# Performance work log

Measured on AMD Instinct MI355X. Metric: run time of the kernel, lower is better.

## Reference

```python
import jax, jax.numpy as jnp
import numpy as np

EPS = 1e-6
LN_EPS = 1e-6

def _mlstm_parallel_stabilized(q, k, v, igate_preact, fgate_preact):
    # q,k,v: (B,NH,S,DH); igate_preact,fgate_preact: (B,NH,S,1)
    B, NH, S, DH = q.shape
    log_fg = jax.nn.log_sigmoid(fgate_preact[..., 0])            # (B,NH,S)
    cs = jnp.cumsum(log_fg, axis=-1)                             # (B,NH,S)
    # log decay matrix: entry (i,j) = cumsum_i - cumsum_j, lower-triangular (j<=i)
    fg_mat = cs[..., :, None] - cs[..., None, :]                 # (B,NH,S,S)
    mask = jnp.tril(jnp.ones((S, S), dtype=bool))
    log_D = jnp.where(mask, fg_mat + igate_preact[..., 0][..., None, :], -jnp.inf)
    max_log_D = jnp.max(log_D, axis=-1, keepdims=True)           # (B,NH,S,1)
    D = jnp.exp(log_D - max_log_D)                               # (B,NH,S,S)
    k_scaled = k / jnp.sqrt(jnp.float32(DH)).astype(k.dtype)
    qk = jnp.einsum('bhsd,bhtd->bhst', q, k_scaled)              # (B,NH,S,S)
    C = qk * D
    normalizer = jnp.maximum(jnp.abs(jnp.sum(C, axis=-1, keepdims=True)), jnp.exp(-max_log_D))
    C_norm = C / (normalizer + EPS)
    return jnp.einsum('bhst,bhtd->bhsd', C_norm, v)              # (B,NH,S,DH)

def _multihead_layernorm(x, weight):
    # x: (B,NH,S,DH), weight: (NH,DH); normalize over DH per head, no bias
    mu = jnp.mean(x, axis=-1, keepdims=True)
    var = jnp.mean(jnp.square(x - mu), axis=-1, keepdims=True)
    xn = (x - mu) * jax.lax.rsqrt(var + LN_EPS)
    return xn * weight[None, :, None, :]

def setup_inputs() -> dict:
    key = jax.random.key(0)
    ks = jax.random.split(key, 6)
    B, S, E, NH = 2, 2048, 1024, 8
    q = jax.random.normal(ks[0], (B, S, E), dtype=jnp.float32)
    k = jax.random.normal(ks[1], (B, S, E), dtype=jnp.float32)
    v = jax.random.normal(ks[2], (B, S, E), dtype=jnp.float32)
    igate_kernel = jnp.zeros((3 * E, NH), dtype=jnp.float32)
    igate_bias = 0.1 * jax.random.normal(ks[3], (NH,), dtype=jnp.float32)
    fgate_kernel = jnp.zeros((3 * E, NH), dtype=jnp.float32)
    fgate_bias = jnp.linspace(3.0, 6.0, NH, dtype=jnp.float32)
    outnorm_weight = jnp.ones((NH, E // NH), dtype=jnp.float32)
    return {"q": q, "k": k, "v": v,
            "igate_kernel": igate_kernel, "igate_bias": igate_bias,
            "fgate_kernel": fgate_kernel, "fgate_bias": fgate_bias,
            "outnorm_weight": outnorm_weight}

def reference(q, k, v, igate_kernel, igate_bias, fgate_kernel, fgate_bias, outnorm_weight):
    B, S, E = q.shape
    NH = igate_bias.shape[0]
    qkv = jnp.concatenate([q, k, v], axis=-1)                    # (B,S,3E)
    igate_preact = qkv @ igate_kernel + igate_bias               # (B,S,NH)
    fgate_preact = qkv @ fgate_kernel + fgate_bias               # (B,S,NH)
    qh = q.reshape(B, S, NH, -1).transpose(0, 2, 1, 3)           # (B,NH,S,DH)
    kh = k.reshape(B, S, NH, -1).transpose(0, 2, 1, 3)
    vh = v.reshape(B, S, NH, -1).transpose(0, 2, 1, 3)
    ig = igate_preact.transpose(0, 2, 1)[..., None]              # (B,NH,S,1)
    fg = fgate_preact.transpose(0, 2, 1)[..., None]
    h = _mlstm_parallel_stabilized(qh, kh, vh, ig, fg)           # (B,NH,S,DH)
    h_norm = _multihead_layernorm(h, outnorm_weight)
    return h_norm.transpose(0, 2, 1, 3).reshape(B, S, -1)        # (B,S,E)
```

## Files before the change

kernel.cpp:

```cpp
#include <hip/hip_runtime.h>
#include <math.h>

#define S_LEN 2048
#define E_DIM 1024
#define NHEAD 8
#define DHEAD 128

typedef short bf16x8 __attribute__((ext_vector_type(8)));
typedef float f32x4 __attribute__((ext_vector_type(4)));
typedef unsigned int u32x4 __attribute__((ext_vector_type(4)));
typedef unsigned int u32x2 __attribute__((ext_vector_type(2)));

constexpr float RSQ_DH  = 0.08838834764831843f;
constexpr float LNRSQ   = -2.4260151319598084f;
constexpr float EPS_NORM = 1e-6f;
constexpr float LN_EPS_C = 1e-6f;

__device__ inline unsigned bfpair(float lo, float hi) {
  unsigned a = __builtin_bit_cast(unsigned, lo);
  unsigned b = __builtin_bit_cast(unsigned, hi);
  a = (a + 0x7fffu + ((a >> 16) & 1u)) >> 16;
  b = (b + 0x7fffu + ((b >> 16) & 1u)) >> 16;
  return a | (b << 16);
}

__device__ inline void gload_lds16(const void* g, void* lds) {
  __builtin_amdgcn_global_load_lds(
      (const __attribute__((address_space(1))) unsigned int*)g,
      (__attribute__((address_space(3))) unsigned int*)lds, 16, 0, 0);
}

__global__ __launch_bounds__(256) void gates_fused(
    const float* __restrict__ q, const float* __restrict__ k, const float* __restrict__ v,
    const float* __restrict__ Wi, const float* __restrict__ bi,
    const float* __restrict__ Wf, const float* __restrict__ bf,
    float* __restrict__ ig_pre, float* __restrict__ fg_pre,
    unsigned short* __restrict__ kb) {
  const int t = threadIdx.x;
  const int row0 = blockIdx.x * 4;
  const int b = row0 >> 11;
  const int s0 = row0 & 2047;
  float p[4][16];
#pragma unroll
  for (int rr = 0; rr < 4; ++rr)
#pragma unroll
    for (int c = 0; c < 16; ++c) p[rr][c] = 0.f;

#pragma unroll
  for (int i = 0; i < 3; ++i) {
    const float* base = (i == 0) ? q : (i == 1) ? k : v;
    float xs[4][4];
#pragma unroll
    for (int rr = 0; rr < 4; ++rr) {
      const float4 xv = *(const float4*)(base + (size_t)(row0 + rr) * E_DIM + t * 4);
      xs[rr][0] = xv.x; xs[rr][1] = xv.y; xs[rr][2] = xv.z; xs[rr][3] = xv.w;
    }
#pragma unroll
    for (int j = 0; j < 4; ++j) {
      const int ge = i * E_DIM + t * 4 + j;
      const float4 wiA = *(const float4*)(Wi + (size_t)ge * 8);
      const float4 wiB = *(const float4*)(Wi + (size_t)ge * 8 + 4);
      const float4 wfA = *(const float4*)(Wf + (size_t)ge * 8);
      const float4 wfB = *(const float4*)(Wf + (size_t)ge * 8 + 4);
      const float wv16[16] = {wiA.x, wiA.y, wiA.z, wiA.w, wiB.x, wiB.y, wiB.z, wiB.w,
                              wfA.x, wfA.y, wfA.z, wfA.w, wfB.x, wfB.y, wfB.z, wfB.w};
#pragma unroll
      for (int rr = 0; rr < 4; ++rr) {
        const float x = xs[rr][j];
#pragma unroll
        for (int c = 0; c < 16; ++c) p[rr][c] += x * wv16[c];
      }
    }
    if (i == 1 && kb != nullptr) {
      const int h = (t * 4) >> 7, d = (t * 4) & 127;
#pragma unroll
      for (int rr = 0; rr < 4; ++rr) {
        u32x2 pk;
        pk.x = bfpair(xs[rr][0], xs[rr][1]);
        pk.y = bfpair(xs[rr][2], xs[rr][3]);
        *(u32x2*)(kb + (((size_t)b * NHEAD + h) * S_LEN + (s0 + rr)) * DHEAD + d) = pk;
      }
    }
  }

#pragma unroll
  for (int rr = 0; rr < 4; ++rr)
#pragma unroll
    for (int c = 0; c < 16; ++c) {
      float val = p[rr][c];
      val += __shfl_xor(val, 1);
      val += __shfl_xor(val, 2);
      val += __shfl_xor(val, 4);
      val += __shfl_xor(val, 8);
      val += __shfl_xor(val, 16);
      val += __shfl_xor(val, 32);
      p[rr][c] = val;
    }
  __shared__ float sred[4][4][16];
  const int wid = t >> 6, lane = t & 63;
  if (lane == 0) {
#pragma unroll
    for (int rr = 0; rr < 4; ++rr)
#pragma unroll
      for (int c = 0; c < 16; ++c) sred[wid][rr][c] = p[rr][c];
  }
  __syncthreads();
  if (t < 64) {
    const int rr = t >> 4, c = t & 15;
    float sum = sred[0][rr][c] + sred[1][rr][c] + sred[2][rr][c] + sred[3][rr][c];
    const int h = c & 7;
    const int row = row0 + rr;
    const int bb = row / S_LEN, s = row % S_LEN;
    if (c < 8) ig_pre[((size_t)bb * NHEAD + h) * S_LEN + s] = sum + bi[h];
    else       fg_pre[((size_t)bb * NHEAD + h) * S_LEN + s] = sum + bf[h];
  }
}

__global__ __launch_bounds__(256) void vtrans(const float* __restrict__ v,
                                              unsigned short* __restrict__ vtb) {
  __shared__ unsigned int tile[128][36];
  const int bid = blockIdx.x;
  const int bh = bid >> 5, st = bid & 31;
  const int b = bh >> 3, h = bh & 7;
  const int s0 = st * 64;
  const int t = threadIdx.x;
#pragma unroll
  for (int i = 0; i < 4; ++i) {
    const int task = t + 256 * i;
    const int sp = task & 31, dq = task >> 5;
    const float* src = v + ((size_t)b * S_LEN + s0 + 2 * sp) * E_DIM + h * DHEAD + dq * 4;
    const float4 r0 = *(const float4*)(src);
    const float4 r1 = *(const float4*)(src + E_DIM);
    tile[dq * 4 + 0][sp] = bfpair(r0.x, r1.x);
    tile[dq * 4 + 1][sp] = bfpair(r0.y, r1.y);
    tile[dq * 4 + 2][sp] = bfpair(r0.z, r1.z);
    tile[dq * 4 + 3][sp] = bfpair(r0.w, r1.w);
  }
  __syncthreads();
#pragma unroll
  for (int i = 0; i < 2; ++i) {
    const int task = t + 256 * i;
    const int d = task >> 2, c4 = task & 3;
    u32x4 w0, w1;
    w0.x = tile[d][c4 * 8 + 0]; w0.y = tile[d][c4 * 8 + 1];
    w0.z = tile[d][c4 * 8 + 2]; w0.w = tile[d][c4 * 8 + 3];
    w1.x = tile[d][c4 * 8 + 4]; w1.y = tile[d][c4 * 8 + 5];
    w1.z = tile[d][c4 * 8 + 6]; w1.w = tile[d][c4 * 8 + 7];
    unsigned short* dst = vtb + ((size_t)bh * DHEAD + d) * S_LEN + s0 + c4 * 16;
    *(u32x4*)(dst)     = w0;
    *(u32x4*)(dst + 8) = w1;
  }
}

__global__ __launch_bounds__(256) void scan_kernel(
    const float* __restrict__ ig_pre, const float* __restrict__ fg_pre,
    float* __restrict__ cs_out, float* __restrict__ g_out, float* __restrict__ gmax_out,
    float g_add) {
  const int bhh = blockIdx.x;
  const int t = threadIdx.x;
  const size_t base = (size_t)bhh * S_LEN;
  float vals[8];
  float run = 0.f;
#pragma unroll
  for (int i = 0; i < 8; ++i) {
    const float x = fg_pre[base + t * 8 + i];
    const float lf = fminf(x, 0.f) - log1pf(__expf(-fabsf(x)));
    run += lf;
    vals[i] = run;
  }
  __shared__ float sums[256];
  sums[t] = run;
  __syncthreads();
  for (int off = 1; off < 256; off <<= 1) {
    const float other = (t >= off) ? sums[t - off] : 0.f;
    __syncthreads();
    sums[t] += other;
    __syncthreads();
  }
  const float prefix = (t > 0) ? sums[t - 1] : 0.f;
  float g_loc[8], gm_loc[8];
  float lmax = -3.4e38f;
#pragma unroll
  for (int i = 0; i < 8; ++i) {
    const float csv = vals[i] + prefix;
    vals[i] = csv;
    const float gg = ig_pre[base + t * 8 + i] - csv;
    g_loc[i] = gg;
    lmax = fmaxf(lmax, gg);
    gm_loc[i] = lmax;
  }
  __shared__ float maxs[256];
  maxs[t] = lmax;
  __syncthreads();
  for (int off = 1; off < 256; off <<= 1) {
    const float other = (t >= off) ? maxs[t - off] : -3.4e38f;
    __syncthreads();
    maxs[t] = fmaxf(maxs[t], other);
    __syncthreads();
  }
  const float pmax = (t > 0) ? maxs[t - 1] : -3.4e38f;
#pragma unroll
  for (int i = 0; i < 8; ++i) {
    cs_out[base + t * 8 + i]   = vals[i];
    g_out[base + t * 8 + i]    = g_loc[i] + g_add;
    gmax_out[base + t * 8 + i] = fmaxf(gm_loc[i], pmax);
  }
}

__global__ __launch_bounds__(128) void mlstm_mfma3(
    const unsigned short* __restrict__ kb, const unsigned short* __restrict__ vtb,
    const float* __restrict__ q,
    const float* __restrict__ cs, const float* __restrict__ garr, const float* __restrict__ gmax,
    const float* __restrict__ wgt, float* __restrict__ out) {
  __shared__ __align__(16) unsigned char kbuf[16384];
  __shared__ __align__(16) unsigned char vbuf[16384];
  __shared__ float g_sh[64];

  const int bid = blockIdx.x;
  const int bh = 2 * (bid & 7) + ((bid >> 3) & 1);
  const int qb = 63 - (bid >> 4);
  const int b = bh >> 3, h = bh & 7;
  const int t = threadIdx.x;
  const int w = t >> 6;
  const int l = t & 63;
  const int r = l & 15;
  const int qq = l >> 4;
  const size_t bhS = (size_t)bh * S_LEN;

  const int gr = qb * 32 + 2 * r + w;
  const float gm_lane = gmax[bhS + gr];

  bf16x8 qfrag[4];
  {
    const float* qrow = q + ((size_t)b * S_LEN + gr) * E_DIM + h * DHEAD;
#pragma unroll
    for (int c = 0; c < 4; ++c) {
      const float4 f0 = *(const float4*)(qrow + 32 * c + 8 * qq);
      const float4 f1 = *(const float4*)(qrow + 32 * c + 8 * qq + 4);
      u32x4 u;
      u.x = bfpair(f0.x, f0.y); u.y = bfpair(f0.z, f0.w);
      u.z = bfpair(f1.x, f1.y); u.w = bfpair(f1.z, f1.w);
      qfrag[c] = __builtin_bit_cast(bf16x8, u);
    }
  }

  f32x4 o[8];
#pragma unroll
  for (int n = 0; n < 8; ++n) o[n] = (f32x4){0.f, 0.f, 0.f, 0.f};
  float den_p = 0.f;

  const unsigned short* kt = kb + bhS * DHEAD;
  const unsigned short* vt = vtb + (size_t)bh * DHEAD * S_LEN;

  const int ntiles = (qb >> 1) + 1;
  for (int jt = 0; jt < ntiles; ++jt) {
    const int j0 = jt * 64;
#pragma unroll
    for (int a = 0; a < 8; ++a) {
      const int m = w * 512 + a * 64 + l;
      const int u = m ^ ((m >> 4) & 7);
      const int j = u >> 4, seg = u & 15;
      gload_lds16(kt + ((size_t)(j0 + j)) * DHEAD + seg * 8,
                  &kbuf[(w * 512 + a * 64) * 16]);
    }
#pragma unroll
    for (int a = 0; a < 8; ++a) {
      const int m = w * 512 + a * 64 + l;
      const int u = m ^ ((m >> 3) & 7);
      const int d = u >> 3, qv = u & 7;
      gload_lds16(vt + (size_t)d * S_LEN + j0 + qv * 8,
                  &vbuf[(w * 512 + a * 64) * 16]);
    }
    if (t < 64) g_sh[t] = garr[bhS + j0 + t];
    asm volatile("s_waitcnt vmcnt(0)" ::: "memory");
    __syncthreads();

    f32x4 st[4];
#pragma unroll
    for (int g = 0; g < 4; ++g) st[g] = (f32x4){0.f, 0.f, 0.f, 0.f};
#pragma unroll
    for (int c = 0; c < 4; ++c) {
#pragma unroll
      for (int g = 0; g < 4; ++g) {
        const int u = ((16 * g + r) * 16 + 4 * c + qq) ^ (r & 7);
        bf16x8 ka = *(const bf16x8*)&kbuf[u * 16];
        st[g] = __builtin_amdgcn_mfma_f32_16x16x32_bf16(ka, qfrag[c], st[g], 0, 0, 0);
      }
    }

    const bool diag = (jt == ntiles - 1);
    unsigned P[4][2];
#pragma unroll
    for (int g = 0; g < 4; ++g) {
      float wv[4];
#pragma unroll
      for (int m = 0; m < 4; ++m) {
        const int jl = 16 * g + 4 * qq + m;
        float ww = st[g][m] * __expf(g_sh[jl] - gm_lane);
        if (diag && (j0 + jl > gr)) ww = 0.f;
        wv[m] = ww;
        den_p += ww;
      }
      P[g][0] = bfpair(wv[0], wv[1]);
      P[g][1] = bfpair(wv[2], wv[3]);
    }

    unsigned A0[4], A1[4];
#pragma unroll
    for (int m = 0; m < 4; ++m) {
      const int srcl = r + 16 * (2 * (qq & 1) + (m >> 1));
      const unsigned x0 = (unsigned)__shfl((int)P[0][m & 1], srcl);
      const unsigned x1 = (unsigned)__shfl((int)P[1][m & 1], srcl);
      const unsigned x2 = (unsigned)__shfl((int)P[2][m & 1], srcl);
      const unsigned x3 = (unsigned)__shfl((int)P[3][m & 1], srcl);
      A0[m] = (qq < 2) ? x0 : x1;
      A1[m] = (qq < 2) ? x2 : x3;
    }
    u32x4 ua0, ua1;
    ua0.x = A0[0]; ua0.y = A0[1]; ua0.z = A0[2]; ua0.w = A0[3];
    ua1.x = A1[0]; ua1.y = A1[1]; ua1.z = A1[2]; ua1.w = A1[3];
    const bf16x8 pa0 = __builtin_bit_cast(bf16x8, ua0);
    const bf16x8 pa1 = __builtin_bit_cast(bf16x8, ua1);

#pragma unroll
    for (int n = 0; n < 8; ++n) {
      const int d = 16 * n + r;
      const int u0 = (d * 8 + qq)     ^ (d & 7);
      const int u1 = (d * 8 + 4 + qq) ^ (d & 7);
      bf16x8 vb0 = *(const bf16x8*)&vbuf[u0 * 16];
      bf16x8 vb1 = *(const bf16x8*)&vbuf[u1 * 16];
      o[n] = __builtin_amdgcn_mfma_f32_16x16x32_bf16(pa0, vb0, o[n], 0, 0, 0);
      o[n] = __builtin_amdgcn_mfma_f32_16x16x32_bf16(pa1, vb1, o[n], 0, 0, 0);
    }
    __syncthreads();
  }

  float den_f = den_p;
  den_f += __shfl_xor(den_f, 16);
  den_f += __shfl_xor(den_f, 32);

  const float* wrow = wgt + h * DHEAD;
  float wv_n[8];
#pragma unroll
  for (int n = 0; n < 8; ++n) wv_n[n] = wrow[16 * n + r];

#pragma unroll
  for (int m = 0; m < 4; ++m) {
    const int iloc = 4 * qq + m;
    const float den_o = __shfl(den_f, iloc);
    const int grow = qb * 32 + 2 * iloc + w;
    const float csg = cs[bhS + grow];
    const float gmg = gmax[bhS + grow];
    const float norm = fmaxf(fabsf(den_o), __expf(-(csg + gmg))) + EPS_NORM;
    const float inv = 1.f / norm;
    float hv[8];
    float s1 = 0.f, s2 = 0.f;
#pragma unroll
    for (int n = 0; n < 8; ++n) {
      hv[n] = o[n][m] * inv;
      s1 += hv[n]; s2 += hv[n] * hv[n];
    }
    s1 += __shfl_xor(s1, 1); s1 += __shfl_xor(s1, 2);
    s1 += __shfl_xor(s1, 4); s1 += __shfl_xor(s1, 8);
    s2 += __shfl_xor(s2, 1); s2 += __shfl_xor(s2, 2);
    s2 += __shfl_xor(s2, 4); s2 += __shfl_xor(s2, 8);
    const float mu  = s1 * (1.f / 128.f);
    const float var = s2 * (1.f / 128.f) - mu * mu;
    const float rstd = rsqrtf(var + LN_EPS_C);
    float* orow = out + ((size_t)b * S_LEN + grow) * E_DIM + h * DHEAD;
#pragma unroll
    for (int n = 0; n < 8; ++n)
      orow[16 * n + r] = (hv[n] - mu) * rstd * wv_n[n];
  }
}

__global__ __launch_bounds__(256) void mlstm_mfma(
    const float* __restrict__ q, const float* __restrict__ k, const float* __restrict__ v,
    const float* __restrict__ cs, const float* __restrict__ garr, const float* __restrict__ gmax,
    const float* __restrict__ wgt, float* __restrict__ out) {
  __shared__ unsigned short k_lds[32][136];
  __shared__ unsigned int   vt_u32[128][20];
  __shared__ unsigned int   xch[4][16][20];
  __shared__ float          g_sh[32];

  const int bid = blockIdx.x;
  int qt;
  if (bid < 256) qt = 31 - (bid >> 4);
  else           qt = (bid - 256) >> 4;
  const int bh = bid & 15;
  const int b = bh >> 3, h = bh & 7;
  const int t = threadIdx.x;
  const int w = t >> 6;
  const int l = t & 63;
  const int r = l & 15;
  const int qq = l >> 4;
  const size_t bhS = (size_t)bh * S_LEN;

  const int gr = qt * 64 + 4 * r + w;
  const float gm_lane = gmax[bhS + gr];

  bf16x8 qfrag[4];
  {
    const float* qrow = q + ((size_t)b * S_LEN + gr) * E_DIM + h * DHEAD;
#pragma unroll
    for (int c = 0; c < 4; ++c) {
      const float4 f0 = *(const float4*)(qrow + 32 * c + 8 * qq);
      const float4 f1 = *(const float4*)(qrow + 32 * c + 8 * qq + 4);
      u32x4 u;
      u.x = bfpair(f0.x, f0.y); u.y = bfpair(f0.z, f0.w);
      u.z = bfpair(f1.x, f1.y); u.w = bfpair(f1.z, f1.w);
      qfrag[c] = __builtin_bit_cast(bf16x8, u);
    }
  }

  f32x4 o[8];
#pragma unroll
  for (int n = 0; n < 8; ++n) o[n] = (f32x4){0.f, 0.f, 0.f, 0.f};
  float den_p = 0.f;

  const int kj = t >> 3, ks = t & 7;
  const int vjp = t & 15, vds = t >> 4;

  const int ntiles = 2 * qt + 2;
  for (int jt = 0; jt < ntiles; ++jt) {
    const int j0 = jt * 32;
    {
      const float* src = k + ((size_t)b * S_LEN + j0 + kj) * E_DIM + h * DHEAD + ks * 16;
      float4 f0 = *(const float4*)(src);
      float4 f1 = *(const float4*)(src + 4);
      float4 f2 = *(const float4*)(src + 8);
      float4 f3 = *(const float4*)(src + 12);
      u32x4 ua, ub;
      ua.x = bfpair(f0.x, f0.y); ua.y = bfpair(f0.z, f0.w);
      ua.z = bfpair(f1.x, f1.y); ua.w = bfpair(f1.z, f1.w);
      ub.x = bfpair(f2.x, f2.y); ub.y = bfpair(f2.z, f2.w);
      ub.z = bfpair(f3.x, f3.y); ub.w = bfpair(f3.z, f3.w);
      *(u32x4*)&k_lds[kj][ks * 16]     = ua;
      *(u32x4*)&k_lds[kj][ks * 16 + 8] = ub;
    }
    {
      const float* s0 = v + ((size_t)b * S_LEN + j0 + 2 * vjp) * E_DIM + h * DHEAD + vds * 8;
      const float* s1 = s0 + E_DIM;
      float4 a0 = *(const float4*)(s0);
      float4 a1 = *(const float4*)(s0 + 4);
      float4 b0 = *(const float4*)(s1);
      float4 b1 = *(const float4*)(s1 + 4);
      vt_u32[vds * 8 + 0][vjp] = bfpair(a0.x, b0.x);
      vt_u32[vds * 8 + 1][vjp] = bfpair(a0.y, b0.y);
      vt_u32[vds * 8 + 2][vjp] = bfpair(a0.z, b0.z);
      vt_u32[vds * 8 + 3][vjp] = bfpair(a0.w, b0.w);
      vt_u32[vds * 8 + 4][vjp] = bfpair(a1.x, b1.x);
      vt_u32[vds * 8 + 5][vjp] = bfpair(a1.y, b1.y);
      vt_u32[vds * 8 + 6][vjp] = bfpair(a1.z, b1.z);
      vt_u32[vds * 8 + 7][vjp] = bfpair(a1.w, b1.w);
    }
    if (t < 32) g_sh[t] = garr[bhS + j0 + t];
    __syncthreads();

    f32x4 st0 = {0, 0, 0, 0}, st1 = {0, 0, 0, 0};
#pragma unroll
    for (int c = 0; c < 4; ++c) {
      bf16x8 ka0 = *(const bf16x8*)&k_lds[r][32 * c + 8 * qq];
      bf16x8 ka1 = *(const bf16x8*)&k_lds[16 + r][32 * c + 8 * qq];
      st0 = __builtin_amdgcn_mfma_f32_16x16x32_bf16(ka0, qfrag[c], st0, 0, 0, 0);
      st1 = __builtin_amdgcn_mfma_f32_16x16x32_bf16(ka1, qfrag[c], st1, 0, 0, 0);
    }

    const bool diag = (jt >= 2 * qt);
    float wv0[4], wv1[4];
#pragma unroll
    for (int reg = 0; reg < 4; ++reg) {
      const int jl0 = 4 * qq + reg, jl1 = 16 + 4 * qq + reg;
      const float e0 = __expf(g_sh[jl0] - gm_lane);
      const float e1 = __expf(g_sh[jl1] - gm_lane);
      float w0 = st0[reg] * RSQ_DH * e0;
      float w1 = st1[reg] * RSQ_DH * e1;
      if (diag) {
        if (j0 + jl0 > gr) w0 = 0.f;
        if (j0 + jl1 > gr) w1 = 0.f;
      }
      wv0[reg] = w0; wv1[reg] = w1;
      den_p += w0 + w1;
    }

    u32x2 p0, p1;
    p0.x = bfpair(wv0[0], wv0[1]); p0.y = bfpair(wv0[2], wv0[3]);
    p1.x = bfpair(wv1[0], wv1[1]); p1.y = bfpair(wv1[2], wv1[3]);
    *(u32x2*)&xch[w][r][2 * qq]     = p0;
    *(u32x2*)&xch[w][r][8 + 2 * qq] = p1;
    __builtin_amdgcn_wave_barrier();
    bf16x8 pa = *(const bf16x8*)&xch[w][r][4 * qq];
    __builtin_amdgcn_wave_barrier();

#pragma unroll
    for (int n = 0; n < 8; ++n) {
      bf16x8 vb = *(const bf16x8*)&vt_u32[16 * n + r][4 * qq];
      o[n] = __builtin_amdgcn_mfma_f32_16x16x32_bf16(pa, vb, o[n], 0, 0, 0);
    }
    __syncthreads();
  }

  float den_f = den_p;
  den_f += __shfl_xor(den_f, 16);
  den_f += __shfl_xor(den_f, 32);

  const float* wrow = wgt + h * DHEAD;
  float wv_n[8];
#pragma unroll
  for (int n = 0; n < 8; ++n) wv_n[n] = wrow[16 * n + r];

#pragma unroll
  for (int reg = 0; reg < 4; ++reg) {
    const int iloc = 4 * qq + reg;
    const float den_o = __shfl(den_f, iloc);
    const int grow = qt * 64 + 4 * iloc + w;
    const float csg = cs[bhS + grow];
    const float gmg = gmax[bhS + grow];
    const float norm = fmaxf(fabsf(den_o), __expf(-(csg + gmg))) + EPS_NORM;
    const float inv = 1.f / norm;
    float hv[8];
    float s1 = 0.f, s2 = 0.f;
#pragma unroll
    for (int n = 0; n < 8; ++n) {
      hv[n] = o[n][reg] * inv;
      s1 += hv[n]; s2 += hv[n] * hv[n];
    }
    s1 += __shfl_xor(s1, 1); s1 += __shfl_xor(s1, 2);
    s1 += __shfl_xor(s1, 4); s1 += __shfl_xor(s1, 8);
    s2 += __shfl_xor(s2, 1); s2 += __shfl_xor(s2, 2);
    s2 += __shfl_xor(s2, 4); s2 += __shfl_xor(s2, 8);
    const float mu  = s1 * (1.f / 128.f);
    const float var = s2 * (1.f / 128.f) - mu * mu;
    const float rstd = rsqrtf(var + LN_EPS_C);
    float* orow = out + ((size_t)b * S_LEN + grow) * E_DIM + h * DHEAD;
#pragma unroll
    for (int n = 0; n < 8; ++n)
      orow[16 * n + r] = (hv[n] - mu) * rstd * wv_n[n];
  }
}

extern "C" void kernel_launch(void* const* d_in, const int* in_sizes, int n_in,
                              void* d_out, int out_size, void* d_ws, size_t ws_size,
                              hipStream_t stream) {
  (void)in_sizes; (void)n_in; (void)out_size;
  const float* q   = (const float*)d_in[0];
  const float* k   = (const float*)d_in[1];
  const float* v   = (const float*)d_in[2];
  const float* Wi  = (const float*)d_in[3];
  const float* bi  = (const float*)d_in[4];
  const float* Wf  = (const float*)d_in[5];
  const float* bf  = (const float*)d_in[6];
  const float* wgt = (const float*)d_in[7];
  float* out = (float*)d_out;
  float* ws  = (float*)d_ws;
  const int BNS = 2 * NHEAD * S_LEN;
  float* ig_pre = ws;
  float* fg_pre = ws + (size_t)BNS;
  float* cs     = ws + (size_t)2 * BNS;
  float* gv     = ws + (size_t)3 * BNS;
  float* gmaxs  = ws + (size_t)4 * BNS;
  unsigned short* kb  = (unsigned short*)(ws + (size_t)5 * BNS);
  unsigned short* vtb = kb + (size_t)16 * S_LEN * DHEAD;

  const size_t need = (size_t)5 * BNS * 4 + (size_t)2 * 16 * S_LEN * DHEAD * 2;

  if (ws_size >= need) {
    gates_fused<<<1024, 256, 0, stream>>>(q, k, v, Wi, bi, Wf, bf, ig_pre, fg_pre, kb);
    vtrans<<<512, 256, 0, stream>>>(v, vtb);
    scan_kernel<<<16, 256, 0, stream>>>(ig_pre, fg_pre, cs, gv, gmaxs, LNRSQ);
    mlstm_mfma3<<<1024, 128, 0, stream>>>(kb, vtb, q, cs, gv, gmaxs, wgt, out);
  } else {
    gates_fused<<<1024, 256, 0, stream>>>(q, k, v, Wi, bi, Wf, bf, ig_pre, fg_pre, nullptr);
    scan_kernel<<<16, 256, 0, stream>>>(ig_pre, fg_pre, cs, gv, gmaxs, 0.0f);
    mlstm_mfma<<<512, 256, 0, stream>>>(q, k, v, cs, gv, gmaxs, wgt, out);
  }
}
```

Baseline: 117.4 us.

## Double-buffer K/V tiles in mLSTM kernel and widen gate rows per block

The main attention kernel now prefetches the next K/V tile and gate values into a second LDS buffer while computing on the current one. It uses a partial vmcnt wait and raises wave priority during the MFMA phase. The gate kernel processes 8 rows per block instead of 4, halving weight reloads. The extra LDS doubles the shared footprint, which may reduce blocks per CU, and the larger gate accumulators raise register pressure.

```diff
diff --git a/kernel.cpp b/kernel.cpp
--- a/kernel.cpp
+++ b/kernel.cpp
@@ -28,6 +28,11 @@
   __builtin_amdgcn_global_load_lds(
       (const __attribute__((address_space(1))) unsigned int*)g,
       (__attribute__((address_space(3))) unsigned int*)lds, 16, 0, 0);
+}
+__device__ inline void gload_lds4(const void* g, void* lds) {
+  __builtin_amdgcn_global_load_lds(
+      (const __attribute__((address_space(1))) unsigned int*)g,
+      (__attribute__((address_space(3))) unsigned int*)lds, 4, 0, 0);
 }
 
 __global__ __launch_bounds__(256) void gates_fused(
@@ -37,21 +42,21 @@
     float* __restrict__ ig_pre, float* __restrict__ fg_pre,
     unsigned short* __restrict__ kb) {
   const int t = threadIdx.x;
-  const int row0 = blockIdx.x * 4;
+  const int row0 = blockIdx.x * 8;
   const int b = row0 >> 11;
   const int s0 = row0 & 2047;
-  float p[4][16];
-#pragma unroll
-  for (int rr = 0; rr < 4; ++rr)
+  float p[8][16];
+#pragma unroll
+  for (int rr = 0; rr < 8; ++rr)
 #pragma unroll
     for (int c = 0; c < 16; ++c) p[rr][c] = 0.f;
 
 #pragma unroll
   for (int i = 0; i < 3; ++i) {
     const float* base = (i == 0) ? q : (i == 1) ? k : v;
-    float xs[4][4];
-#pragma unroll
-    for (int rr = 0; rr < 4; ++rr) {
+    float xs[8][4];
+#pragma unroll
+    for (int rr = 0; rr < 8; ++rr) {
       const float4 xv = *(const float4*)(base + (size_t)(row0 + rr) * E_DIM + t * 4);
       xs[rr][0] = xv.x; xs[rr][1] = xv.y; xs[rr][2] = xv.z; xs[rr][3] = xv.w;
     }
@@ -65,7 +70,7 @@
       const float wv16[16] = {wiA.x, wiA.y, wiA.z, wiA.w, wiB.x, wiB.y, wiB.z, wiB.w,
                               wfA.x, wfA.y, wfA.z, wfA.w, wfB.x, wfB.y, wfB.z, wfB.w};
 #pragma unroll
-      for (int rr = 0; rr < 4; ++rr) {
+      for (int rr = 0; rr < 8; ++rr) {
         const float x = xs[rr][j];
 #pragma unroll
         for (int c = 0; c < 16; ++c) p[rr][c] += x * wv16[c];
@@ -74,7 +79,7 @@
     if (i == 1 && kb != nullptr) {
       const int h = (t * 4) >> 7, d = (t * 4) & 127;
 #pragma unroll
-      for (int rr = 0; rr < 4; ++rr) {
+      for (int rr = 0; rr < 8; ++rr) {
         u32x2 pk;
         pk.x = bfpair(xs[rr][0], xs[rr][1]);
         pk.y = bfpair(xs[rr][2], xs[rr][3]);
@@ -84,7 +89,7 @@
   }
 
 #pragma unroll
-  for (int rr = 0; rr < 4; ++rr)
+  for (int rr = 0; rr < 8; ++rr)
 #pragma unroll
     for (int c = 0; c < 16; ++c) {
       float val = p[rr][c];
@@ -96,16 +101,16 @@
       val += __shfl_xor(val, 32);
       p[rr][c] = val;
     }
-  __shared__ float sred[4][4][16];
+  __shared__ float sred[4][8][16];
   const int wid = t >> 6, lane = t & 63;
   if (lane == 0) {
 #pragma unroll
-    for (int rr = 0; rr < 4; ++rr)
+    for (int rr = 0; rr < 8; ++rr)
 #pragma unroll
       for (int c = 0; c < 16; ++c) sred[wid][rr][c] = p[rr][c];
   }
   __syncthreads();
-  if (t < 64) {
+  if (t < 128) {
     const int rr = t >> 4, c = t & 15;
     float sum = sred[0][rr][c] + sred[1][rr][c] + sred[2][rr][c] + sred[3][rr][c];
     const int h = c & 7;
@@ -212,9 +217,9 @@
     const float* __restrict__ q,
     const float* __restrict__ cs, const float* __restrict__ garr, const float* __restrict__ gmax,
     const float* __restrict__ wgt, float* __restrict__ out) {
-  __shared__ __align__(16) unsigned char kbuf[16384];
-  __shared__ __align__(16) unsigned char vbuf[16384];
-  __shared__ float g_sh[64];
+  __shared__ __align__(16) unsigned char kbuf[2][16384];
+  __shared__ __align__(16) unsigned char vbuf[2][16384];
+  __shared__ float g_sh[2][64];
 
   const int bid = blockIdx.x;
   const int bh = 2 * (bid & 7) + ((bid >> 3) & 1);
@@ -253,15 +258,16 @@
   const unsigned short* vt = vtb + (size_t)bh * DHEAD * S_LEN;
 
   const int ntiles = (qb >> 1) + 1;
-  for (int jt = 0; jt < ntiles; ++jt) {
-    const int j0 = jt * 64;
+
+  auto stage = [&](int jt_, int bufi) {
+    const int j0 = jt_ * 64;
 #pragma unroll
     for (int a = 0; a < 8; ++a) {
       const int m = w * 512 + a * 64 + l;
       const int u = m ^ ((m >> 4) & 7);
       const int j = u >> 4, seg = u & 15;
       gload_lds16(kt + ((size_t)(j0 + j)) * DHEAD + seg * 8,
-                  &kbuf[(w * 512 + a * 64) * 16]);
+                  &kbuf[bufi][(w * 512 + a * 64) * 16]);
     }
 #pragma unroll
     for (int a = 0; a < 8; ++a) {
@@ -269,11 +275,25 @@
       const int u = m ^ ((m >> 3) & 7);
       const int d = u >> 3, qv = u & 7;
       gload_lds16(vt + (size_t)d * S_LEN + j0 + qv * 8,
-                  &vbuf[(w * 512 + a * 64) * 16]);
-    }
-    if (t < 64) g_sh[t] = garr[bhS + j0 + t];
-    asm volatile("s_waitcnt vmcnt(0)" ::: "memory");
-    __syncthreads();
+                  &vbuf[bufi][(w * 512 + a * 64) * 16]);
+    }
+    gload_lds4(garr + bhS + j0 + l, &g_sh[bufi][0]);
+  };
+
+  stage(0, 0);
+
+  for (int jt = 0; jt < ntiles; ++jt) {
+    const int cur = jt & 1;
+    if (jt + 1 < ntiles) {
+      stage(jt + 1, cur ^ 1);
+      asm volatile("s_waitcnt vmcnt(17)" ::: "memory");
+    } else {
+      asm volatile("s_waitcnt vmcnt(0)" ::: "memory");
+    }
+    __builtin_amdgcn_sched_barrier(0);
+    __syncthreads();
+    __builtin_amdgcn_s_setprio(1);
+    const int j0 = jt * 64;
 
     f32x4 st[4];
 #pragma unroll
@@ -283,7 +303,7 @@
 #pragma unroll
       for (int g = 0; g < 4; ++g) {
         const int u = ((16 * g + r) * 16 + 4 * c + qq) ^ (r & 7);
-        bf16x8 ka = *(const bf16x8*)&kbuf[u * 16];
+        bf16x8 ka = *(const bf16x8*)&kbuf[cur][u * 16];
         st[g] = __builtin_amdgcn_mfma_f32_16x16x32_bf16(ka, qfrag[c], st[g], 0, 0, 0);
       }
     }
@@ -296,7 +316,7 @@
 #pragma unroll
       for (int m = 0; m < 4; ++m) {
         const int jl = 16 * g + 4 * qq + m;
-        float ww = st[g][m] * __expf(g_sh[jl] - gm_lane);
+        float ww = st[g][m] * __expf(g_sh[cur][jl] - gm_lane);
         if (diag && (j0 + jl > gr)) ww = 0.f;
         wv[m] = ww;
         den_p += ww;
@@ -327,11 +347,12 @@
       const int d = 16 * n + r;
       const int u0 = (d * 8 + qq)     ^ (d & 7);
       const int u1 = (d * 8 + 4 + qq) ^ (d & 7);
-      bf16x8 vb0 = *(const bf16x8*)&vbuf[u0 * 16];
-      bf16x8 vb1 = *(const bf16x8*)&vbuf[u1 * 16];
+      bf16x8 vb0 = *(const bf16x8*)&vbuf[cur][u0 * 16];
+      bf16x8 vb1 = *(const bf16x8*)&vbuf[cur][u1 * 16];
       o[n] = __builtin_amdgcn_mfma_f32_16x16x32_bf16(pa0, vb0, o[n], 0, 0, 0);
       o[n] = __builtin_amdgcn_mfma_f32_16x16x32_bf16(pa1, vb1, o[n], 0, 0, 0);
     }
+    __builtin_amdgcn_s_setprio(0);
     __syncthreads();
   }
 
@@ -565,12 +586,12 @@
   const size_t need = (size_t)5 * BNS * 4 + (size_t)2 * 16 * S_LEN * DHEAD * 2;
 
   if (ws_size >= need) {
-    gates_fused<<<1024, 256, 0, stream>>>(q, k, v, Wi, bi, Wf, bf, ig_pre, fg_pre, kb);
+    gates_fused<<<512, 256, 0, stream>>>(q, k, v, Wi, bi, Wf, bf, ig_pre, fg_pre, kb);
     vtrans<<<512, 256, 0, stream>>>(v, vtb);
     scan_kernel<<<16, 256, 0, stream>>>(ig_pre, fg_pre, cs, gv, gmaxs, LNRSQ);
     mlstm_mfma3<<<1024, 128, 0, stream>>>(kb, vtb, q, cs, gv, gmaxs, wgt, out);
   } else {
-    gates_fused<<<1024, 256, 0, stream>>>(q, k, v, Wi, bi, Wf, bf, ig_pre, fg_pre, nullptr);
+    gates_fused<<<512, 256, 0, stream>>>(q, k, v, Wi, bi, Wf, bf, ig_pre, fg_pre, nullptr);
     scan_kernel<<<16, 256, 0, stream>>>(ig_pre, fg_pre, cs, gv, gmaxs, 0.0f);
     mlstm_mfma<<<512, 256, 0, stream>>>(q, k, v, cs, gv, gmaxs, wgt, out);
   }
```

Result: no change. 116.9 us (-0.4%).

## Restructure mLSTM attention kernel into 8-wave blocks with double-buffered split-K tiles

Applied to the files above, without the earlier changes.

The main attention kernel is replaced by a 512-thread version. Each block handles 64 query rows, and two groups of four waves split each 64-key tile into 32-key halves. Loads for the next tile go through global_load_lds into a double buffer while the current tile is computed, with a partial vmcnt wait in place of a full drain. The two halves' partial outputs and denominators are reduced through LDS before the normalization and layernorm epilogue. It also switches bf16 packing to the hardware v_cvt_pk_bf16_f32 instruction, adds s_setprio around the MFMA sections, and balances block scheduling by pairing long and short causal rows. The aim is to hide global-load latency and raise MFMA utilization, at the cost of a bigger LDS footprint, an extra reduction step, and a hand-tuned vmcnt count that has to match the number of issued loads.

```diff
diff --git a/kernel.cpp b/kernel.cpp
--- a/kernel.cpp
+++ b/kernel.cpp
@@ -24,10 +24,21 @@
   return a | (b << 16);
 }
 
+__device__ inline unsigned cvtpk(float lo, float hi) {
+  unsigned r;
+  asm("v_cvt_pk_bf16_f32 %0, %1, %2" : "=v"(r) : "v"(lo), "v"(hi));
+  return r;
+}
+
 __device__ inline void gload_lds16(const void* g, void* lds) {
   __builtin_amdgcn_global_load_lds(
       (const __attribute__((address_space(1))) unsigned int*)g,
       (__attribute__((address_space(3))) unsigned int*)lds, 16, 0, 0);
+}
+__device__ inline void gload_lds4(const void* g, void* lds) {
+  __builtin_amdgcn_global_load_lds(
+      (const __attribute__((address_space(1))) unsigned int*)g,
+      (__attribute__((address_space(3))) unsigned int*)lds, 4, 0, 0);
 }
 
 __global__ __launch_bounds__(256) void gates_fused(
@@ -207,27 +218,33 @@
   }
 }
 
-__global__ __launch_bounds__(128) void mlstm_mfma3(
+__global__ __launch_bounds__(512, 4) void mlstm_mfma8(
     const unsigned short* __restrict__ kb, const unsigned short* __restrict__ vtb,
     const float* __restrict__ q,
     const float* __restrict__ cs, const float* __restrict__ garr, const float* __restrict__ gmax,
     const float* __restrict__ wgt, float* __restrict__ out) {
-  __shared__ __align__(16) unsigned char kbuf[16384];
-  __shared__ __align__(16) unsigned char vbuf[16384];
-  __shared__ float g_sh[64];
+  __shared__ __align__(16) unsigned char kbuf[4][8192];
+  __shared__ __align__(16) unsigned char vbuf[4][8192];
+  __shared__ float g_sh[4][32];
+  __shared__ float den_sh[4][64];
 
   const int bid = blockIdx.x;
-  const int bh = 2 * (bid & 7) + ((bid >> 3) & 1);
-  const int qb = 63 - (bid >> 4);
+  int qb;
+  if (bid < 256) qb = 31 - (bid >> 4);
+  else           qb = (bid - 256) >> 4;
+  const int g16 = bid & 15;
+  const int bh = 2 * (g16 & 7) + (g16 >> 3);
   const int b = bh >> 3, h = bh & 7;
   const int t = threadIdx.x;
   const int w = t >> 6;
+  const int ig = w & 3;
+  const int tp = w >> 2;
   const int l = t & 63;
   const int r = l & 15;
   const int qq = l >> 4;
   const size_t bhS = (size_t)bh * S_LEN;
 
-  const int gr = qb * 32 + 2 * r + w;
+  const int gr = qb * 64 + 4 * r + ig;
   const float gm_lane = gmax[bhS + gr];
 
   bf16x8 qfrag[4];
@@ -252,125 +269,150 @@
   const unsigned short* kt = kb + bhS * DHEAD;
   const unsigned short* vt = vtb + (size_t)bh * DHEAD * S_LEN;
 
-  const int ntiles = (qb >> 1) + 1;
-  for (int jt = 0; jt < ntiles; ++jt) {
-    const int j0 = jt * 64;
-#pragma unroll
-    for (int a = 0; a < 8; ++a) {
-      const int m = w * 512 + a * 64 + l;
+  auto stage = [&](int pair, int set) {
+    const int j0 = pair * 64 + tp * 32;
+    const int bi = set * 2 + tp;
+#pragma unroll
+    for (int a = 0; a < 2; ++a) {
+      const int m = ig * 128 + a * 64 + l;
       const int u = m ^ ((m >> 4) & 7);
-      const int j = u >> 4, seg = u & 15;
-      gload_lds16(kt + ((size_t)(j0 + j)) * DHEAD + seg * 8,
-                  &kbuf[(w * 512 + a * 64) * 16]);
-    }
-#pragma unroll
-    for (int a = 0; a < 8; ++a) {
-      const int m = w * 512 + a * 64 + l;
+      gload_lds16(kt + ((size_t)(j0 + (u >> 4))) * DHEAD + (u & 15) * 8,
+                  &kbuf[bi][(ig * 128 + a * 64) * 16]);
+    }
+#pragma unroll
+    for (int a = 0; a < 2; ++a) {
+      const int m = ig * 128 + a * 64 + l;
       const int u = m ^ ((m >> 3) & 7);
-      const int d = u >> 3, qv = u & 7;
-      gload_lds16(vt + (size_t)d * S_LEN + j0 + qv * 8,
-                  &vbuf[(w * 512 + a * 64) * 16]);
-    }
-    if (t < 64) g_sh[t] = garr[bhS + j0 + t];
-    asm volatile("s_waitcnt vmcnt(0)" ::: "memory");
-    __syncthreads();
-
-    f32x4 st[4];
-#pragma unroll
-    for (int g = 0; g < 4; ++g) st[g] = (f32x4){0.f, 0.f, 0.f, 0.f};
+      gload_lds16(vt + (size_t)(u >> 2) * S_LEN + j0 + (u & 3) * 8,
+                  &vbuf[bi][(ig * 128 + a * 64) * 16]);
+    }
+    if (l < 32) gload_lds4(garr + bhS + j0 + l, &g_sh[bi][0]);
+  };
+
+  auto body = [&](int j0, int bi, bool diag) {
+    __builtin_amdgcn_s_setprio(1);
+    f32x4 st0 = {0, 0, 0, 0}, st1 = {0, 0, 0, 0};
 #pragma unroll
     for (int c = 0; c < 4; ++c) {
-#pragma unroll
-      for (int g = 0; g < 4; ++g) {
-        const int u = ((16 * g + r) * 16 + 4 * c + qq) ^ (r & 7);
-        bf16x8 ka = *(const bf16x8*)&kbuf[u * 16];
-        st[g] = __builtin_amdgcn_mfma_f32_16x16x32_bf16(ka, qfrag[c], st[g], 0, 0, 0);
+      const int u0 = ((r)      * 16 + 4 * c + qq) ^ (r & 7);
+      const int u1 = ((16 + r) * 16 + 4 * c + qq) ^ (r & 7);
+      bf16x8 ka0 = *(const bf16x8*)&kbuf[bi][u0 * 16];
+      bf16x8 ka1 = *(const bf16x8*)&kbuf[bi][u1 * 16];
+      st0 = __builtin_amdgcn_mfma_f32_16x16x32_bf16(ka0, qfrag[c], st0, 0, 0, 0);
+      st1 = __builtin_amdgcn_mfma_f32_16x16x32_bf16(ka1, qfrag[c], st1, 0, 0, 0);
+    }
+    __builtin_amdgcn_s_setprio(0);
+
+    unsigned P0[2], P1[2];
+    {
+      float wv[4];
+#pragma unroll
+      for (int m = 0; m < 4; ++m) {
+        const int jl = 4 * qq + m;
+        float ww = st0[m] * __expf(g_sh[bi][jl] - gm_lane);
+        if (diag && (j0 + jl > gr)) ww = 0.f;
+        wv[m] = ww; den_p += ww;
       }
-    }
-
-    const bool diag = (jt == ntiles - 1);
-    unsigned P[4][2];
-#pragma unroll
-    for (int g = 0; g < 4; ++g) {
-      float wv[4];
+      P0[0] = cvtpk(wv[0], wv[1]); P0[1] = cvtpk(wv[2], wv[3]);
 #pragma unroll
       for (int m = 0; m < 4; ++m) {
-        const int jl = 16 * g + 4 * qq + m;
-        float ww = st[g][m] * __expf(g_sh[jl] - gm_lane);
+        const int jl = 16 + 4 * qq + m;
+        float ww = st1[m] * __expf(g_sh[bi][jl] - gm_lane);
         if (diag && (j0 + jl > gr)) ww = 0.f;
-        wv[m] = ww;
-        den_p += ww;
+        wv[m] = ww; den_p += ww;
       }
-      P[g][0] = bfpair(wv[0], wv[1]);
-      P[g][1] = bfpair(wv[2], wv[3]);
-    }
-
-    unsigned A0[4], A1[4];
+      P1[0] = cvtpk(wv[0], wv[1]); P1[1] = cvtpk(wv[2], wv[3]);
+    }
+
+    unsigned A0[4];
 #pragma unroll
     for (int m = 0; m < 4; ++m) {
       const int srcl = r + 16 * (2 * (qq & 1) + (m >> 1));
-      const unsigned x0 = (unsigned)__shfl((int)P[0][m & 1], srcl);
-      const unsigned x1 = (unsigned)__shfl((int)P[1][m & 1], srcl);
-      const unsigned x2 = (unsigned)__shfl((int)P[2][m & 1], srcl);
-      const unsigned x3 = (unsigned)__shfl((int)P[3][m & 1], srcl);
+      const unsigned x0 = (unsigned)__shfl((int)P0[m & 1], srcl);
+      const unsigned x1 = (unsigned)__shfl((int)P1[m & 1], srcl);
       A0[m] = (qq < 2) ? x0 : x1;
-      A1[m] = (qq < 2) ? x2 : x3;
-    }
-    u32x4 ua0, ua1;
-    ua0.x = A0[0]; ua0.y = A0[1]; ua0.z = A0[2]; ua0.w = A0[3];
-    ua1.x = A1[0]; ua1.y = A1[1]; ua1.z = A1[2]; ua1.w = A1[3];
-    const bf16x8 pa0 = __builtin_bit_cast(bf16x8, ua0);
-    const bf16x8 pa1 = __builtin_bit_cast(bf16x8, ua1);
-
+    }
+    u32x4 ua;
+    ua.x = A0[0]; ua.y = A0[1]; ua.z = A0[2]; ua.w = A0[3];
+    const bf16x8 pa = __builtin_bit_cast(bf16x8, ua);
+
+    __builtin_amdgcn_s_setprio(1);
 #pragma unroll
     for (int n = 0; n < 8; ++n) {
-      const int d = 16 * n + r;
-      const int u0 = (d * 8 + qq)     ^ (d & 7);
-      const int u1 = (d * 8 + 4 + qq) ^ (d & 7);
-      bf16x8 vb0 = *(const bf16x8*)&vbuf[u0 * 16];
-      bf16x8 vb1 = *(const bf16x8*)&vbuf[u1 * 16];
-      o[n] = __builtin_amdgcn_mfma_f32_16x16x32_bf16(pa0, vb0, o[n], 0, 0, 0);
-      o[n] = __builtin_amdgcn_mfma_f32_16x16x32_bf16(pa1, vb1, o[n], 0, 0, 0);
-    }
-    __syncthreads();
-  }
-
-  float den_f = den_p;
-  den_f += __shfl_xor(den_f, 16);
-  den_f += __shfl_xor(den_f, 32);
-
-  const float* wrow = wgt + h * DHEAD;
-  float wv_n[8];
-#pragma unroll
-  for (int n = 0; n < 8; ++n) wv_n[n] = wrow[16 * n + r];
-
-#pragma unroll
-  for (int m = 0; m < 4; ++m) {
-    const int iloc = 4 * qq + m;
-    const float den_o = __shfl(den_f, iloc);
-    const int grow = qb * 32 + 2 * iloc + w;
-    const float csg = cs[bhS + grow];
-    const float gmg = gmax[bhS + grow];
-    const float norm = fmaxf(fabsf(den_o), __expf(-(csg + gmg))) + EPS_NORM;
-    const float inv = 1.f / norm;
-    float hv[8];
-    float s1 = 0.f, s2 = 0.f;
-#pragma unroll
-    for (int n = 0; n < 8; ++n) {
-      hv[n] = o[n][m] * inv;
-      s1 += hv[n]; s2 += hv[n] * hv[n];
-    }
-    s1 += __shfl_xor(s1, 1); s1 += __shfl_xor(s1, 2);
-    s1 += __shfl_xor(s1, 4); s1 += __shfl_xor(s1, 8);
-    s2 += __shfl_xor(s2, 1); s2 += __shfl_xor(s2, 2);
-    s2 += __shfl_xor(s2, 4); s2 += __shfl_xor(s2, 8);
-    const float mu  = s1 * (1.f / 128.f);
-    const float var = s2 * (1.f / 128.f) - mu * mu;
-    const float rstd = rsqrtf(var + LN_EPS_C);
-    float* orow = out + ((size_t)b * S_LEN + grow) * E_DIM + h * DHEAD;
+      const int ud = (16 * n + r) * 4 + qq;
+      const int up = ud ^ ((ud >> 3) & 7);
+      bf16x8 vb = *(const bf16x8*)&vbuf[bi][up * 16];
+      o[n] = __builtin_amdgcn_mfma_f32_16x16x32_bf16(pa, vb, o[n], 0, 0, 0);
+    }
+    __builtin_amdgcn_s_setprio(0);
+  };
+
+  stage(0, 0);
+  for (int p = 0; p < qb; ++p) {
+    stage(p + 1, (p + 1) & 1);
+    asm volatile("s_waitcnt vmcnt(5)" ::: "memory");
+    __builtin_amdgcn_sched_barrier(0);
+    __syncthreads();
+    body(p * 64 + tp * 32, (p & 1) * 2 + tp, false);
+    __syncthreads();
+  }
+  asm volatile("s_waitcnt vmcnt(0)" ::: "memory");
+  __builtin_amdgcn_sched_barrier(0);
+  __syncthreads();
+  body(qb * 64 + tp * 32, (qb & 1) * 2 + tp, true);
+
+  float* osh = (float*)&kbuf[0][0];
+  __syncthreads();
+  if (tp == 1) {
 #pragma unroll
     for (int n = 0; n < 8; ++n)
-      orow[16 * n + r] = (hv[n] - mu) * rstd * wv_n[n];
+      *(f32x4*)&osh[(((n << 2) + ig) * 64 + l) * 4] = o[n];
+    den_sh[ig][l] = den_p;
+  }
+  __syncthreads();
+  if (tp == 0) {
+    den_p += den_sh[ig][l];
+#pragma unroll
+    for (int n = 0; n < 8; ++n)
+      o[n] += *(const f32x4*)&osh[(((n << 2) + ig) * 64 + l) * 4];
+
+    float den_f = den_p;
+    den_f += __shfl_xor(den_f, 16);
+    den_f += __shfl_xor(den_f, 32);
+
+    const float* wrow = wgt + h * DHEAD;
+    float wv_n[8];
+#pragma unroll
+    for (int n = 0; n < 8; ++n) wv_n[n] = wrow[16 * n + r];
+
+#pragma unroll
+    for (int m = 0; m < 4; ++m) {
+      const int iloc = 4 * qq + m;
+      const float den_o = __shfl(den_f, iloc);
+      const int grow = qb * 64 + 4 * iloc + ig;
+      const float csg = cs[bhS + grow];
+      const float gmg = gmax[bhS + grow];
+      const float norm = fmaxf(fabsf(den_o), __expf(-(csg + gmg))) + EPS_NORM;
+      const float inv = 1.f / norm;
+      float hv[8];
+      float s1 = 0.f, s2 = 0.f;
+#pragma unroll
+      for (int n = 0; n < 8; ++n) {
+        hv[n] = o[n][m] * inv;
+        s1 += hv[n]; s2 += hv[n] * hv[n];
+      }
+      s1 += __shfl_xor(s1, 1); s1 += __shfl_xor(s1, 2);
+      s1 += __shfl_xor(s1, 4); s1 += __shfl_xor(s1, 8);
+      s2 += __shfl_xor(s2, 1); s2 += __shfl_xor(s2, 2);
+      s2 += __shfl_xor(s2, 4); s2 += __shfl_xor(s2, 8);
+      const float mu  = s1 * (1.f / 128.f);
+      const float var = s2 * (1.f / 128.f) - mu * mu;
+      const float rstd = rsqrtf(var + LN_EPS_C);
+      float* orow = out + ((size_t)b * S_LEN + grow) * E_DIM + h * DHEAD;
+#pragma unroll
+      for (int n = 0; n < 8; ++n)
+        orow[16 * n + r] = (hv[n] - mu) * rstd * wv_n[n];
+    }
   }
 }
 
@@ -568,7 +610,7 @@
     gates_fused<<<1024, 256, 0, stream>>>(q, k, v, Wi, bi, Wf, bf, ig_pre, fg_pre, kb);
     vtrans<<<512, 256, 0, stream>>>(v, vtb);
     scan_kernel<<<16, 256, 0, stream>>>(ig_pre, fg_pre, cs, gv, gmaxs, LNRSQ);
-    mlstm_mfma3<<<1024, 128, 0, stream>>>(kb, vtb, q, cs, gv, gmaxs, wgt, out);
+    mlstm_mfma8<<<512, 512, 0, stream>>>(kb, vtb, q, cs, gv, gmaxs, wgt, out);
   } else {
     gates_fused<<<1024, 256, 0, stream>>>(q, k, v, Wi, bi, Wf, bf, ig_pre, fg_pre, nullptr);
     scan_kernel<<<16, 256, 0, stream>>>(ig_pre, fg_pre, cs, gv, gmaxs, 0.0f);
```

After: 106.6 us. 9.2% less time.
